# Optimization experiments

Hardware: AMD Instinct MI355X
Metric: run time of the kernel (lower is better)

## Reference

```python
import jax, jax.numpy as jnp
import numpy as np

BS, N, HEADS, DIN, DOUT = 512, 128, 8, 64, 64


def setup_inputs() -> dict:
    key = jax.random.key(0)
    k1, k2, k3, k4, k5 = jax.random.split(key, 5)
    h = jax.random.normal(k1, (BS, N, DIN), dtype=jnp.float32)
    w = jax.random.normal(k2, (HEADS, DIN, DOUT), dtype=jnp.float32) * 0.1
    a_src = jax.random.normal(k3, (HEADS, DOUT, 1), dtype=jnp.float32) * 0.1
    a_dst = jax.random.normal(k4, (HEADS, DOUT, 1), dtype=jnp.float32) * 0.1
    bias = jnp.zeros((DOUT,), dtype=jnp.float32)
    # sparse random adjacency with self-loops so every softmax row is valid
    adj = jax.random.uniform(k5, (BS, N, N)) < 0.05
    adj = adj | jnp.eye(N, dtype=bool)[None, :, :]
    return {"h": h, "adj": adj, "w": w, "a_src": a_src, "a_dst": a_dst, "bias": bias}


def reference(h, adj, w, a_src, a_dst, bias):
    # h: [b, n, i]; w: [H, i, o] -> h_prime: [b, H, n, o]
    h_prime = jnp.einsum('bni,hio->bhno', h, w)
    t = jnp.tanh(h_prime)
    attn_src = jnp.einsum('bhno,ho->bhn', t, a_src[..., 0])  # [b, H, n]
    attn_dst = jnp.einsum('bhno,ho->bhn', t, a_dst[..., 0])  # [b, H, n]
    # attn[b,h,i,j] = src[b,h,i] + dst[b,h,j]
    attn = attn_src[..., :, None] + attn_dst[..., None, :]
    attn = jax.nn.leaky_relu(attn, negative_slope=0.2)
    attn = jnp.where(adj[:, None, :, :], attn, -jnp.inf)
    attn = jax.nn.softmax(attn, axis=-1)
    out = jnp.einsum('bhij,bhjo->bhio', attn, h_prime)
    return out + bias
```

## Files before the change

kernel.cpp:

```cpp
#include <hip/hip_runtime.h>

#define BSZ 512
#define NN 128
#define HEADS 8
#define DIN 64
#define DOUT 64

typedef __bf16 bf16x8 __attribute__((ext_vector_type(8)));
typedef float floatx4 __attribute__((ext_vector_type(4)));

static __device__ __forceinline__ unsigned short f2bf(float f) {
    __bf16 b = (__bf16)f;
    return __builtin_bit_cast(unsigned short, b);
}
static __device__ __forceinline__ bf16x8 ld_frag(const unsigned short* p) {
    uint4 r = *reinterpret_cast<const uint4*>(p);
    return __builtin_bit_cast(bf16x8, r);
}

__global__ __launch_bounds__(512) void prep(
    const int* __restrict__ adj, const float* __restrict__ w,
    unsigned int* __restrict__ msk, unsigned short* __restrict__ wT, int do_w)
{
    const int b = blockIdx.x;
    const int t = threadIdx.x;
    const int* ap = adj + (size_t)b * NN * NN + (t >> 2) * NN + (t & 3) * 32;
    unsigned int m = 0;
    #pragma unroll
    for (int q = 0; q < 8; ++q) {
        int4 v = *reinterpret_cast<const int4*>(ap + q * 4);
        m |= (v.x != 0 ? (1u << (4 * q + 0)) : 0u)
           | (v.y != 0 ? (1u << (4 * q + 1)) : 0u)
           | (v.z != 0 ? (1u << (4 * q + 2)) : 0u)
           | (v.w != 0 ? (1u << (4 * q + 3)) : 0u);
    }
    msk[b * 512 + t] = m;

    if (do_w && b < HEADS) {
        const float* wg = w + b * DIN * DOUT;
        const int o = t >> 3, k0 = (t & 7) * 8;
        unsigned int u[4];
        #pragma unroll
        for (int p = 0; p < 4; ++p) {
            float f0 = wg[(k0 + 2 * p) * DOUT + o];
            float f1 = wg[(k0 + 2 * p + 1) * DOUT + o];
            u[p] = f2bf(f0) | ((unsigned int)f2bf(f1) << 16);
        }
        *reinterpret_cast<uint4*>(&wT[b * DOUT * DIN + o * DIN + k0]) =
            make_uint4(u[0], u[1], u[2], u[3]);
    }
}

__global__ __launch_bounds__(512, 6) void gat_fwd(
    const float* __restrict__ hin,
    const unsigned int* __restrict__ mskg,
    const unsigned short* __restrict__ wTg,
    const float* __restrict__ w,
    const float* __restrict__ a_src,
    const float* __restrict__ a_dst,
    const float* __restrict__ bias,
    float* __restrict__ out)
{
    __shared__ __attribute__((aligned(16))) unsigned short hpT[DOUT * NN];
    __shared__ __attribute__((aligned(16))) unsigned short P[NN * NN];
    __shared__ __attribute__((aligned(16))) float s_src[NN];
    __shared__ __attribute__((aligned(16))) float s_dst[NN];

    const int bid  = blockIdx.x;
    const int b    = bid >> 3;
    const int hd   = bid & 7;
    const int tid  = threadIdx.x;
    const int lane = tid & 63;
    const int wv   = tid >> 6;
    const int lg   = lane >> 4;
    const int lm   = lane & 15;
    const int n0   = wv * 16;

    const float* hb = hin + (size_t)b * NN * DIN;
    bf16x8 hA[2];
    #pragma unroll
    for (int kt = 0; kt < 2; ++kt) {
        const float* p = hb + (n0 + lm) * DIN + kt * 32 + lg * 8;
        float4 v0 = *reinterpret_cast<const float4*>(p);
        float4 v1 = *reinterpret_cast<const float4*>(p + 4);
        bf16x8 a;
        a[0] = (__bf16)v0.x; a[1] = (__bf16)v0.y; a[2] = (__bf16)v0.z; a[3] = (__bf16)v0.w;
        a[4] = (__bf16)v1.x; a[5] = (__bf16)v1.y; a[6] = (__bf16)v1.z; a[7] = (__bf16)v1.w;
        hA[kt] = a;
    }
    const unsigned int mw = mskg[b * 512 + (n0 + lm) * 4 + lg];

    floatx4 acc[4] = {floatx4{0,0,0,0}, floatx4{0,0,0,0}, floatx4{0,0,0,0}, floatx4{0,0,0,0}};
    if (wTg) {
        const unsigned short* wt = wTg + hd * DOUT * DIN;
        #pragma unroll
        for (int kt = 0; kt < 2; ++kt) {
            #pragma unroll
            for (int nt = 0; nt < 4; ++nt) {
                bf16x8 bfr = ld_frag(&wt[(nt * 16 + lm) * DIN + kt * 32 + lg * 8]);
                acc[nt] = __builtin_amdgcn_mfma_f32_16x16x32_bf16(hA[kt], bfr, acc[nt], 0, 0, 0);
            }
        }
    } else {
        const float* wg = w + hd * DIN * DOUT;
        #pragma unroll
        for (int kt = 0; kt < 2; ++kt) {
            #pragma unroll
            for (int nt = 0; nt < 4; ++nt) {
                const float* wp = wg + (kt * 32 + lg * 8) * DOUT + nt * 16 + lm;
                bf16x8 bfr;
                #pragma unroll
                for (int q = 0; q < 8; ++q) bfr[q] = (__bf16)wp[q * DOUT];
                acc[nt] = __builtin_amdgcn_mfma_f32_16x16x32_bf16(hA[kt], bfr, acc[nt], 0, 0, 0);
            }
        }
    }
    const float* asp = a_src + hd * DOUT;
    const float* adp = a_dst + hd * DOUT;
    float ps[4] = {0, 0, 0, 0}, pd[4] = {0, 0, 0, 0};
    #pragma unroll
    for (int nt = 0; nt < 4; ++nt) {
        const int o = nt * 16 + lm;
        const float as = asp[o], ad = adp[o];
        #pragma unroll
        for (int r = 0; r < 4; ++r) {
            const float v = acc[nt][r];
            const float ex = __expf(2.f * v);
            const float t = 1.f - 2.f / (ex + 1.f);
            ps[r] = fmaf(t, as, ps[r]);
            pd[r] = fmaf(t, ad, pd[r]);
        }
        const int jb = n0 + lg * 4;
        unsigned int u01 = f2bf(acc[nt][0]) | ((unsigned int)f2bf(acc[nt][1]) << 16);
        unsigned int u23 = f2bf(acc[nt][2]) | ((unsigned int)f2bf(acc[nt][3]) << 16);
        const int base = (o * 128 + jb) ^ ((o & 7) << 3);
        *reinterpret_cast<unsigned int*>(&hpT[base])     = u01;
        *reinterpret_cast<unsigned int*>(&hpT[base + 2]) = u23;
    }
    #pragma unroll
    for (int r = 0; r < 4; ++r) {
        #pragma unroll
        for (int m = 1; m <= 8; m <<= 1) {
            ps[r] += __shfl_xor(ps[r], m);
            pd[r] += __shfl_xor(pd[r], m);
        }
    }
    if (lm == 0) {
        #pragma unroll
        for (int r = 0; r < 4; ++r) {
            s_src[n0 + lg * 4 + r] = ps[r];
            s_dst[n0 + lg * 4 + r] = pd[r];
        }
    }
    __syncthreads();

    const int i = n0 + lm;
    const int sw = (i & 7) << 3;
    const float si = s_src[i];

    const int pz = i * 128 + lg * 32;
    #pragma unroll
    for (int t = 0; t < 4; ++t)
        *reinterpret_cast<uint4*>(&P[(pz + 8 * t) ^ sw]) = make_uint4(0, 0, 0, 0);

    unsigned int m = mw;
    float sum = 0.f;
    while (m) {
        const int q = __builtin_ctz(m); m &= m - 1;
        const float x = si + s_dst[lg * 32 + q];
        const float xl = fmaxf(x, 0.f) + 0.2f * fminf(x, 0.f);
        const float e = __expf(xl);
        const __bf16 eb = (__bf16)e;
        sum += (float)eb;
        P[(pz + q) ^ sw] = __builtin_bit_cast(unsigned short, eb);
    }
    sum += __shfl_xor(sum, 16);
    sum += __shfl_xor(sum, 32);
    const float inv = 1.f / sum;

    floatx4 oacc[4] = {floatx4{0,0,0,0}, floatx4{0,0,0,0}, floatx4{0,0,0,0}, floatx4{0,0,0,0}};
    #pragma unroll
    for (int kt = 0; kt < 4; ++kt) {
        const bf16x8 af = ld_frag(&P[(i * 128 + kt * 32 + lg * 8) ^ sw]);
        #pragma unroll
        for (int nt = 0; nt < 4; ++nt) {
            const int o = nt * 16 + lm;
            bf16x8 bfr = ld_frag(&hpT[(o * 128 + kt * 32 + lg * 8) ^ ((o & 7) << 3)]);
            oacc[nt] = __builtin_amdgcn_mfma_f32_16x16x32_bf16(bfr, af, oacc[nt], 0, 0, 0);
        }
    }
    float* outr = out + (((size_t)b * HEADS + hd) * NN + (n0 + lm)) * DOUT;
    #pragma unroll
    for (int nt = 0; nt < 4; ++nt) {
        const float4 bv = *reinterpret_cast<const float4*>(&bias[nt * 16 + lg * 4]);
        float4 st;
        st.x = fmaf(oacc[nt][0], inv, bv.x);
        st.y = fmaf(oacc[nt][1], inv, bv.y);
        st.z = fmaf(oacc[nt][2], inv, bv.z);
        st.w = fmaf(oacc[nt][3], inv, bv.w);
        *reinterpret_cast<float4*>(&outr[nt * 16 + lg * 4]) = st;
    }
}

extern "C" void kernel_launch(void* const* d_in, const int* in_sizes, int n_in,
                              void* d_out, int out_size, void* d_ws, size_t ws_size,
                              hipStream_t stream) {
    (void)in_sizes; (void)n_in; (void)out_size;
    const float* h     = (const float*)d_in[0];
    const int*   adj   = (const int*)d_in[1];
    const float* w     = (const float*)d_in[2];
    const float* a_src = (const float*)d_in[3];
    const float* a_dst = (const float*)d_in[4];
    const float* bias  = (const float*)d_in[5];
    float* out = (float*)d_out;

    unsigned int* msk = (unsigned int*)d_ws;
    const size_t MSK_BYTES = (size_t)BSZ * 512 * 4;
    unsigned short* wT = nullptr;
    const bool use_wt = ws_size >= MSK_BYTES + (size_t)HEADS * DOUT * DIN * 2;
    if (use_wt) wT = (unsigned short*)((char*)d_ws + MSK_BYTES);

    prep<<<dim3(BSZ), dim3(512), 0, stream>>>(adj, w, msk, wT, use_wt ? 1 : 0);
    gat_fwd<<<dim3(BSZ * HEADS), dim3(512), 0, stream>>>(h, msk, wT, w, a_src, a_dst, bias, out);
}
```

Baseline: 81.79 us.

## Build attention P fragments in registers instead of shared memory

```diff
diff --git a/kernel.cpp b/kernel.cpp
--- a/kernel.cpp
+++ b/kernel.cpp
@@ -51,7 +51,7 @@
     }
 }
 
-__global__ __launch_bounds__(512, 6) void gat_fwd(
+__global__ __launch_bounds__(512, 8) void gat_fwd(
     const float* __restrict__ hin,
     const unsigned int* __restrict__ mskg,
     const unsigned short* __restrict__ wTg,
@@ -62,7 +62,6 @@
     float* __restrict__ out)
 {
     __shared__ __attribute__((aligned(16))) unsigned short hpT[DOUT * NN];
-    __shared__ __attribute__((aligned(16))) unsigned short P[NN * NN];
     __shared__ __attribute__((aligned(16))) float s_src[NN];
     __shared__ __attribute__((aligned(16))) float s_dst[NN];
 
@@ -88,7 +87,8 @@
         a[4] = (__bf16)v1.x; a[5] = (__bf16)v1.y; a[6] = (__bf16)v1.z; a[7] = (__bf16)v1.w;
         hA[kt] = a;
     }
-    const unsigned int mw = mskg[b * 512 + (n0 + lm) * 4 + lg];
+    const uint4 mr = *reinterpret_cast<const uint4*>(&mskg[(size_t)b * 512 + (n0 + lm) * 4]);
+    unsigned int mwv[4] = {mr.x, mr.y, mr.z, mr.w};
 
     floatx4 acc[4] = {floatx4{0,0,0,0}, floatx4{0,0,0,0}, floatx4{0,0,0,0}, floatx4{0,0,0,0}};
     if (wTg) {
@@ -155,24 +155,28 @@
     __syncthreads();
 
     const int i = n0 + lm;
-    const int sw = (i & 7) << 3;
     const float si = s_src[i];
 
-    const int pz = i * 128 + lg * 32;
-    #pragma unroll
-    for (int t = 0; t < 4; ++t)
-        *reinterpret_cast<uint4*>(&P[(pz + 8 * t) ^ sw]) = make_uint4(0, 0, 0, 0);
-
-    unsigned int m = mw;
     float sum = 0.f;
-    while (m) {
-        const int q = __builtin_ctz(m); m &= m - 1;
-        const float x = si + s_dst[lg * 32 + q];
-        const float xl = fmaxf(x, 0.f) + 0.2f * fminf(x, 0.f);
-        const float e = __expf(xl);
-        const __bf16 eb = (__bf16)e;
-        sum += (float)eb;
-        P[(pz + q) ^ sw] = __builtin_bit_cast(unsigned short, eb);
+    bf16x8 pf[4];
+    #pragma unroll
+    for (int kt = 0; kt < 4; ++kt) {
+        unsigned long long d01 = 0ull, d23 = 0ull;
+        unsigned int byte = (mwv[kt] >> (lg * 8)) & 0xffu;
+        while (byte) {
+            const int q = __builtin_ctz(byte); byte &= byte - 1;
+            const float x = si + s_dst[kt * 32 + lg * 8 + q];
+            const float xl = fmaxf(x, 0.f) + 0.2f * fminf(x, 0.f);
+            const float e = __expf(xl);
+            const __bf16 eb = (__bf16)e;
+            sum += (float)eb;
+            const unsigned long long v =
+                (unsigned long long)__builtin_bit_cast(unsigned short, eb) << ((q & 3) * 16);
+            if (q < 4) d01 |= v; else d23 |= v;
+        }
+        const uint4 ui = make_uint4((unsigned)d01, (unsigned)(d01 >> 32),
+                                    (unsigned)d23, (unsigned)(d23 >> 32));
+        pf[kt] = __builtin_bit_cast(bf16x8, ui);
     }
     sum += __shfl_xor(sum, 16);
     sum += __shfl_xor(sum, 32);
@@ -181,24 +185,23 @@
     floatx4 oacc[4] = {floatx4{0,0,0,0}, floatx4{0,0,0,0}, floatx4{0,0,0,0}, floatx4{0,0,0,0}};
     #pragma unroll
     for (int kt = 0; kt < 4; ++kt) {
-        const bf16x8 af = ld_frag(&P[(i * 128 + kt * 32 + lg * 8) ^ sw]);
         #pragma unroll
         for (int nt = 0; nt < 4; ++nt) {
             const int o = nt * 16 + lm;
             bf16x8 bfr = ld_frag(&hpT[(o * 128 + kt * 32 + lg * 8) ^ ((o & 7) << 3)]);
-            oacc[nt] = __builtin_amdgcn_mfma_f32_16x16x32_bf16(bfr, af, oacc[nt], 0, 0, 0);
-        }
-    }
-    float* outr = out + (((size_t)b * HEADS + hd) * NN + (n0 + lm)) * DOUT;
+            oacc[nt] = __builtin_amdgcn_mfma_f32_16x16x32_bf16(bfr, pf[kt], oacc[nt], 0, 0, 0);
+        }
+    }
+    float* outr = out + (((size_t)b * HEADS + hd) * NN + i) * DOUT;
     #pragma unroll
     for (int nt = 0; nt < 4; ++nt) {
         const float4 bv = *reinterpret_cast<const float4*>(&bias[nt * 16 + lg * 4]);
-        float4 st;
-        st.x = fmaf(oacc[nt][0], inv, bv.x);
-        st.y = fmaf(oacc[nt][1], inv, bv.y);
-        st.z = fmaf(oacc[nt][2], inv, bv.z);
-        st.w = fmaf(oacc[nt][3], inv, bv.w);
-        *reinterpret_cast<float4*>(&outr[nt * 16 + lg * 4]) = st;
+        floatx4 st;
+        st[0] = fmaf(oacc[nt][0], inv, bv.x);
+        st[1] = fmaf(oacc[nt][1], inv, bv.y);
+        st[2] = fmaf(oacc[nt][2], inv, bv.z);
+        st[3] = fmaf(oacc[nt][3], inv, bv.w);
+        __builtin_nontemporal_store(st, reinterpret_cast<floatx4*>(&outr[nt * 16 + lg * 4]));
     }
 }
 
```

After: 78.80 us. -3.6%, faster.
